# Performance work log

Measured on AMD Instinct MI355X. Metric: run time of the kernel, lower is better.

## Reference

```python
import jax, jax.numpy as jnp
import numpy as np


def setup_inputs() -> dict:
    key = jax.random.key(0)
    ks = jax.random.split(key, 4)
    C = 64
    return {
        "x": jax.random.normal(ks[0], (8, 64, 32, 32, 96), jnp.float32),
        "w_sr": jax.random.normal(ks[1], (64,), jnp.float32) * 0.1,
        "b_sr": jnp.zeros((64,), jnp.float32),
        "Wq": jax.random.normal(ks[2], (64, 64), jnp.float32) / np.sqrt(C),
        "bq": jnp.zeros((64,), jnp.float32),
        "Wkv": jax.random.normal(ks[3], (128, 64), jnp.float32) / np.sqrt(C),
        "bkv": jnp.zeros((128,), jnp.float32),
        "gamma": jnp.ones((4,), jnp.float32),
        "beta": jnp.zeros((4,), jnp.float32),
    }


def reference(x, w_sr, b_sr, Wq, bq, Wkv, bkv, gamma, beta):
    B, C, H, W, D = x.shape
    NH = gamma.shape[0]
    hd = C // NH
    scale = hd ** -0.5

    # 1x1x1 conv projections == channel matmuls
    q = jnp.einsum('oc,bchwd->bohwd', Wq, x) + bq[None, :, None, None, None]
    # sr_conv with sr_ratio=1 is a depthwise 1x1x1 conv: per-channel scale+shift
    kvin = x * w_sr[None, :, None, None, None] + b_sr[None, :, None, None, None]
    kv = jnp.einsum('oc,bchwd->bohwd', Wkv, kvin) + bkv[None, :, None, None, None]
    k, v = kv[:, :C], kv[:, C:]

    q = q.reshape(B, NH, hd, H, W, D)
    k = k.reshape(B, NH, hd, H, W, D)
    v = v.reshape(B, NH, hd, H, W, D)

    # Manhattan decay: spatial_dist[i,j] = |i-j| + |j-i| = 2|i-j| (H==W);
    # spectral_dist is identically zero in the original (d_idx.T is a no-op on 1D).
    idx = jnp.arange(H, dtype=x.dtype)
    dist = 2.0 * jnp.abs(idx[:, None] - idx[None, :])              # (H, H)
    dec = dist[None, :, :, None] * gamma[:, None, None, None] + beta[:, None, None, None]  # (NH,H,H,1)
    decay = jnp.exp(-jax.nn.softplus(dec))                          # broadcasts over D

    # matmul contracts over W; head_dim c is batch-like (faithful to original permutes)
    attn = jnp.einsum('bnchwd,bncgwd->bnchgd', q, k) * scale        # (B,NH,hd,H,H,D)
    attn = attn + decay[None, :, None]                               # (1,NH,1,H,H,1)
    attn = jax.nn.softmax(attn, axis=-1)                             # softmax over spectral D
    out = jnp.einsum('bnchgd,bncgjd->bnchjd', attn, v)               # (B,NH,hd,H,W,D)
    return out.reshape(B, C, H, W, D)
```

## Files before the change

kernel.cpp:

```cpp
#include <hip/hip_runtime.h>
#include <stdint.h>
#include <stddef.h>

typedef __attribute__((ext_vector_type(8))) short short8;
typedef __attribute__((ext_vector_type(4))) float f32x4;

#define PER_BO 98304
#define CSTRIDE 8192

__device__ __forceinline__ unsigned int cvtpk(float lo, float hi) {
    unsigned int r;
    asm("v_cvt_pk_bf16_f32 %0, %1, %2" : "=v"(r) : "v"(lo), "v"(hi));
    return r;
}

__global__ __launch_bounds__(512, 2) void proj_mfma(
    const float* __restrict__ x, const float* __restrict__ w_sr, const float* __restrict__ b_sr,
    const float* __restrict__ Wq, const float* __restrict__ bq,
    const float* __restrict__ Wkv, const float* __restrict__ bkv,
    unsigned short* __restrict__ qb, unsigned short* __restrict__ kb, unsigned short* __restrict__ vb)
{
    __shared__ unsigned short Wh[12288];
    __shared__ float bl[192];
    __shared__ unsigned short Cb[2 * 6464];

    int t = threadIdx.x;
    int bidx = blockIdx.x;
    int b = bidx >> 8;
    int blk = bidx & 255;

    int lane = t & 63;
    int wvi = t >> 6;
    int lr = lane & 15, hk = lane >> 4;

    const float* xb = x + (size_t)b * 6291456 + (size_t)blk * 384;
    float af[3][16];
#pragma unroll
    for (int pi = 0; pi < 3; ++pi) {
        int pt = wvi * 3 + pi;
        const float* xp = xb + (size_t)(hk * 8) * 98304 + pt * 16 + lr;
#pragma unroll
        for (int j = 0; j < 8; ++j) {
            af[pi][j]     = xp[(size_t)j * 98304];
            af[pi][8 + j] = xp[(size_t)(32 + j) * 98304];
        }
    }

#pragma unroll
    for (int i = 0; i < 6; ++i) {
        int qi = t + i * 512;
        int o = qi >> 4;
        int cq = qi & 15;
        int c = cq * 4;
        float4 wv4;
        if (o < 64) wv4 = *reinterpret_cast<const float4*>(Wq + o * 64 + c);
        else {
            wv4 = *reinterpret_cast<const float4*>(Wkv + (o - 64) * 64 + c);
            float4 sr = *reinterpret_cast<const float4*>(w_sr + c);
            wv4.x *= sr.x; wv4.y *= sr.y; wv4.z *= sr.z; wv4.w *= sr.w;
        }
        uint2 pk; pk.x = cvtpk(wv4.x, wv4.y); pk.y = cvtpk(wv4.z, wv4.w);
        int sw = (cq >> 1) ^ (o & 7);
        *reinterpret_cast<uint2*>(&Wh[o * 64 + sw * 8 + (cq & 1) * 4]) = pk;
    }
    if (t < 192) {
        float s;
        if (t < 64) s = bq[t];
        else {
            s = bkv[t - 64];
            for (int c = 0; c < 64; ++c) s += Wkv[(t - 64) * 64 + c] * b_sr[c];
        }
        bl[t] = s;
    }
    __syncthreads();

    short8 ahf[3][2], alf[3][2];
#pragma unroll
    for (int pi = 0; pi < 3; ++pi) {
#pragma unroll
        for (int half = 0; half < 2; ++half) {
            union { unsigned int u[4]; short8 v; } H, L;
#pragma unroll
            for (int q = 0; q < 4; ++q) {
                float f0 = af[pi][half * 8 + 2 * q];
                float f1 = af[pi][half * 8 + 2 * q + 1];
                unsigned int hp = cvtpk(f0, f1);
                float h0 = __uint_as_float(hp << 16);
                float h1 = __uint_as_float(hp & 0xffff0000u);
                H.u[q] = hp;
                L.u[q] = cvtpk(f0 - h0, f1 - h1);
            }
            ahf[pi][half] = H.v; alf[pi][half] = L.v;
        }
    }

    int wo[3];
#pragma unroll
    for (int pi = 0; pi < 3; ++pi) {
        int p0 = (wvi * 3 + pi) * 16 + hk * 4;
        int hwl = p0 / 96;
        int d0 = p0 - hwl * 96;
        wo[pi] = lr * 404 + hwl * 100 + d0;
    }

    int so_po[3], so_lo[3];
#pragma unroll
    for (int i = 0; i < 3; ++i) {
        int flat = i * 512 + t;
        int dlq = flat & 1;
        int hwl = (flat >> 1) & 3;
        int ch  = (flat >> 3) % 12;
        int o   = flat / 96;
        so_po[i] = o * PER_BO + ch * 8192 + (blk * 4 + hwl) * 8 + dlq * 4;
        so_lo[i] = o * 404 + hwl * 100 + ch * 8 + dlq * 4;
    }

    float biasv[12];
#pragma unroll
    for (int ot = 0; ot < 12; ++ot) biasv[ot] = bl[ot * 16 + lr];

    f32x4 zero4 = {0.f, 0.f, 0.f, 0.f};
    int s7 = lr & 7;

#pragma unroll
    for (int ot = 0; ot < 12; ++ot) {
        unsigned short* cb = Cb + (ot & 1) * 6464;
        {
            int o = ot * 16 + lr;
            const unsigned short* wr = &Wh[o * 64];
            short8 b0 = *reinterpret_cast<const short8*>(wr + ((hk ^ s7) * 8));
            short8 b1 = *reinterpret_cast<const short8*>(wr + (((hk + 4) ^ s7) * 8));
            float bo = biasv[ot];
#pragma unroll
            for (int pi = 0; pi < 3; ++pi) {
                f32x4 acc = __builtin_amdgcn_mfma_f32_16x16x32_bf16(ahf[pi][0], b0, zero4, 0, 0, 0);
                acc = __builtin_amdgcn_mfma_f32_16x16x32_bf16(ahf[pi][1], b1, acc, 0, 0, 0);
                acc = __builtin_amdgcn_mfma_f32_16x16x32_bf16(alf[pi][0], b0, acc, 0, 0, 0);
                acc = __builtin_amdgcn_mfma_f32_16x16x32_bf16(alf[pi][1], b1, acc, 0, 0, 0);
                uint2 st;
                st.x = cvtpk(acc[0] + bo, acc[1] + bo);
                st.y = cvtpk(acc[2] + bo, acc[3] + bo);
                *reinterpret_cast<uint2*>(&cb[wo[pi]]) = st;
            }
        }
        __syncthreads();
        {
            int sel = ot >> 2;
            unsigned short* base =
                (sel == 0 ? qb : (sel == 1 ? kb : vb)) + (size_t)(b * 64 + (ot & 3) * 16) * PER_BO;
#pragma unroll
            for (int i = 0; i < 3; ++i)
                *reinterpret_cast<uint2*>(base + so_po[i]) =
                    *reinterpret_cast<const uint2*>(&cb[so_lo[i]]);
        }
    }
}

__global__ __launch_bounds__(512, 4) void attn_kernel(
    const unsigned short* __restrict__ qb, const unsigned short* __restrict__ kb,
    const unsigned short* __restrict__ vb,
    const float* __restrict__ gamma, const float* __restrict__ beta,
    float* __restrict__ out)
{
    extern __shared__ char smem[];
    unsigned short* Qs = (unsigned short*)smem;
    unsigned short* Ks = (unsigned short*)(smem + 17408);
    float* lred = (float*)smem;
    float* rlb  = (float*)(smem + 16896);
    unsigned short* Vs = (unsigned short*)smem;
    float* Osf  = (float*)(smem + 34816);

    int t = threadIdx.x;
    int l = t & 63;
    int dsub = t >> 6;
    int lr = l & 15, hk = l >> 4;

    int id = blockIdx.x;
    int xcd = id & 7;
    int k7 = id >> 3;
    int p = xcd + 8 * (k7 >> 1);
    int half = k7 & 1;
    int oc = p & 63;
    int b = p >> 6;
    int n = oc >> 4;

    const unsigned short* qp = qb + (size_t)(b * 64 + oc) * PER_BO + half * 4096;
    const unsigned short* kp = kb + (size_t)(b * 64 + oc) * PER_BO;
    const unsigned short* vp = vb + (size_t)(b * 64 + oc) * PER_BO;

    float gm = gamma[n], bt = beta[n];
    float decv[8];
#pragma unroll
    for (int gb = 0; gb < 2; ++gb)
#pragma unroll
        for (int r = 0; r < 4; ++r) {
            int hh = half * 16 + hk * 4 + r;
            int gg = gb * 16 + lr;
            float dc = 2.0f * fabsf((float)(hh - gg)) * gm + bt;
            float sp = fmaxf(dc, 0.0f) + log1pf(__expf(-fabsf(dc)));
            decv[gb * 4 + r] = __expf(-sp);
        }

    const float scale = 0.25f;
    f32x4 zero4 = {0.f, 0.f, 0.f, 0.f};

    unsigned int ep[48];
    float lacc[8] = {0.f, 0.f, 0.f, 0.f, 0.f, 0.f, 0.f, 0.f};

    auto WRQ = [&](int buf, uint4 v) {
        const unsigned short* sq = (const unsigned short*)&v;
        int base = buf * 4352 + (t >> 5) * 34 + (t & 31);
#pragma unroll
        for (int i = 0; i < 8; ++i) Qs[base + i * 544] = sq[i];
    };
    auto WRK = [&](int buf, uint4 v0, uint4 v1) {
        const unsigned short* s0 = (const unsigned short*)&v0;
        const unsigned short* s1 = (const unsigned short*)&v1;
        int b0 = buf * 8704 + (t >> 5) * 34 + (t & 31);
        int b1 = buf * 8704 + ((t + 512) >> 5) * 34 + (t & 31);
#pragma unroll
        for (int i = 0; i < 8; ++i) { Ks[b0 + i * 1088] = s0[i]; Ks[b1 + i * 1088] = s1[i]; }
    };

    uint4 qh  = *reinterpret_cast<const uint4*>(qp + t * 8);
    uint4 kh0 = *reinterpret_cast<const uint4*>(kp + t * 8);
    uint4 kh1 = *reinterpret_cast<const uint4*>(kp + (t + 512) * 8);
    WRQ(0, qh); WRK(0, kh0, kh1);
    qh  = *reinterpret_cast<const uint4*>(qp + CSTRIDE + t * 8);
    kh0 = *reinterpret_cast<const uint4*>(kp + CSTRIDE + t * 8);
    kh1 = *reinterpret_cast<const uint4*>(kp + CSTRIDE + (t + 512) * 8);
    __syncthreads();

#pragma unroll
    for (int ch = 0; ch < 12; ++ch) {
        const unsigned short* qbase = Qs + (ch & 1) * 4352 + dsub * 544;
        const unsigned short* kbase = Ks + (ch & 1) * 8704 + dsub * 1088;
        short8 a  = *reinterpret_cast<const short8*>(qbase + lr * 34 + hk * 8);
        short8 b0 = *reinterpret_cast<const short8*>(kbase + lr * 34 + hk * 8);
        short8 b1 = *reinterpret_cast<const short8*>(kbase + (16 + lr) * 34 + hk * 8);
        f32x4 s0 = __builtin_amdgcn_mfma_f32_16x16x32_bf16(a, b0, zero4, 0, 0, 0);
        f32x4 s1 = __builtin_amdgcn_mfma_f32_16x16x32_bf16(a, b1, zero4, 0, 0, 0);
        float e[8];
#pragma unroll
        for (int r = 0; r < 4; ++r) {
            e[r]     = __expf(s0[r] * scale + decv[r]);
            e[4 + r] = __expf(s1[r] * scale + decv[4 + r]);
        }
#pragma unroll
        for (int i = 0; i < 8; ++i) lacc[i] += e[i];
        ep[ch * 4 + 0] = cvtpk(e[0], e[1]);
        ep[ch * 4 + 1] = cvtpk(e[2], e[3]);
        ep[ch * 4 + 2] = cvtpk(e[4], e[5]);
        ep[ch * 4 + 3] = cvtpk(e[6], e[7]);
        if (ch < 11) {
            WRQ((ch + 1) & 1, qh); WRK((ch + 1) & 1, kh0, kh1);
            if (ch < 10) {
                qh  = *reinterpret_cast<const uint4*>(qp + (ch + 2) * CSTRIDE + t * 8);
                kh0 = *reinterpret_cast<const uint4*>(kp + (ch + 2) * CSTRIDE + t * 8);
                kh1 = *reinterpret_cast<const uint4*>(kp + (ch + 2) * CSTRIDE + (t + 512) * 8);
            }
        }
        __syncthreads();
    }

#pragma unroll
    for (int i = 0; i < 8; ++i)
        lred[dsub * 528 + (hk * 4 + (i & 3)) * 33 + (i >> 2) * 16 + lr] = lacc[i];
    __syncthreads();
    {
        float rsum = 0.f;
#pragma unroll
        for (int s = 0; s < 8; ++s) rsum += lred[s * 528 + (t >> 5) * 33 + (t & 31)];
        rlb[(t >> 5) * 33 + (t & 31)] = 1.0f / rsum;
    }
    __syncthreads();
    float rl8[8];
#pragma unroll
    for (int i = 0; i < 8; ++i)
        rl8[i] = rlb[(hk * 4 + (i & 3)) * 33 + (i >> 2) * 16 + lr];
    __syncthreads();

    auto WRV = [&](int buf, uint4 v0, uint4 v1) {
        const unsigned short* s0 = (const unsigned short*)&v0;
        const unsigned short* s1 = (const unsigned short*)&v1;
        int a0 = buf * 8704 + (t & 31) * 34 + (t >> 5);
        int a1 = buf * 8704 + (t & 31) * 34 + (t >> 5) + 16;
#pragma unroll
        for (int i = 0; i < 8; ++i) { Vs[a0 + i * 1088] = s0[i]; Vs[a1 + i * 1088] = s1[i]; }
    };

    uint4 vh0 = *reinterpret_cast<const uint4*>(vp + t * 8);
    uint4 vh1 = *reinterpret_cast<const uint4*>(vp + (t + 512) * 8);
    WRV(0, vh0, vh1);
    vh0 = *reinterpret_cast<const uint4*>(vp + CSTRIDE + t * 8);
    vh1 = *reinterpret_cast<const uint4*>(vp + CSTRIDE + (t + 512) * 8);
    __syncthreads();

    unsigned short* Pb = (unsigned short*)(Osf + dsub * 528);
    size_t obase0 = ((size_t)(b * 64 + oc) * 1024 + half * 512 + t) * 96;
    float4 hA, hB;

#pragma unroll
    for (int ch = 0; ch < 12; ++ch) {
#pragma unroll
        for (int gb = 0; gb < 2; ++gb)
#pragma unroll
            for (int rp = 0; rp < 2; ++rp) {
                unsigned int u = ep[ch * 4 + gb * 2 + rp];
                float p0 = __uint_as_float(u << 16)         * rl8[gb * 4 + rp * 2];
                float p1 = __uint_as_float(u & 0xffff0000u) * rl8[gb * 4 + rp * 2 + 1];
                unsigned int pk = cvtpk(p0, p1);
                Pb[(hk * 4 + rp * 2) * 36 + gb * 16 + lr]     = (unsigned short)pk;
                Pb[(hk * 4 + rp * 2 + 1) * 36 + gb * 16 + lr] = (unsigned short)(pk >> 16);
            }
        asm volatile("s_waitcnt lgkmcnt(0)" ::: "memory");
        __builtin_amdgcn_sched_barrier(0);
        short8 pa = *reinterpret_cast<const short8*>(Pb + lr * 36 + hk * 8);
        const unsigned short* vbase = Vs + (ch & 1) * 8704 + dsub * 1088;
        short8 vb0 = *reinterpret_cast<const short8*>(vbase + lr * 34 + hk * 8);
        short8 vb1 = *reinterpret_cast<const short8*>(vbase + (16 + lr) * 34 + hk * 8);
        f32x4 o0 = __builtin_amdgcn_mfma_f32_16x16x32_bf16(pa, vb0, zero4, 0, 0, 0);
        f32x4 o1 = __builtin_amdgcn_mfma_f32_16x16x32_bf16(pa, vb1, zero4, 0, 0, 0);
        if (ch < 11) {
            WRV((ch + 1) & 1, vh0, vh1);
            if (ch < 10) {
                vh0 = *reinterpret_cast<const uint4*>(vp + (ch + 2) * CSTRIDE + t * 8);
                vh1 = *reinterpret_cast<const uint4*>(vp + (ch + 2) * CSTRIDE + (t + 512) * 8);
            }
        }
#pragma unroll
        for (int r = 0; r < 4; ++r) {
            Osf[dsub * 528 + (hk * 4 + r) * 33 + lr]      = o0[r];
            Osf[dsub * 528 + (hk * 4 + r) * 33 + 16 + lr] = o1[r];
        }
        __syncthreads();
        {
            int lidx = (t >> 5) * 33 + (t & 31);
            float4 cA, cB;
            cA.x = Osf[0 * 528 + lidx]; cA.y = Osf[1 * 528 + lidx];
            cA.z = Osf[2 * 528 + lidx]; cA.w = Osf[3 * 528 + lidx];
            cB.x = Osf[4 * 528 + lidx]; cB.y = Osf[5 * 528 + lidx];
            cB.z = Osf[6 * 528 + lidx]; cB.w = Osf[7 * 528 + lidx];
            if ((ch & 1) == 0) { hA = cA; hB = cB; }
            else {
                float* po = out + obase0 + (ch >> 1) * 16;
                *reinterpret_cast<float4*>(po)      = hA;
                *reinterpret_cast<float4*>(po + 4)  = hB;
                *reinterpret_cast<float4*>(po + 8)  = cA;
                *reinterpret_cast<float4*>(po + 12) = cB;
            }
        }
        __syncthreads();
    }
}

extern "C" void kernel_launch(void* const* d_in, const int* in_sizes, int n_in,
                              void* d_out, int out_size, void* d_ws, size_t ws_size,
                              hipStream_t stream) {
    const float* x     = (const float*)d_in[0];
    const float* w_sr  = (const float*)d_in[1];
    const float* b_sr  = (const float*)d_in[2];
    const float* Wq    = (const float*)d_in[3];
    const float* bq    = (const float*)d_in[4];
    const float* Wkv   = (const float*)d_in[5];
    const float* bkv   = (const float*)d_in[6];
    const float* gamma = (const float*)d_in[7];
    const float* beta  = (const float*)d_in[8];
    float* out = (float*)d_out;

    unsigned short* qb = (unsigned short*)d_ws;
    unsigned short* kb = qb + (size_t)50331648;
    unsigned short* vb = kb + (size_t)50331648;

    proj_mfma<<<2048, 512, 0, stream>>>(x, w_sr, b_sr, Wq, bq, Wkv, bkv, qb, kb, vb);

    (void)hipFuncSetAttribute(reinterpret_cast<const void*>(attn_kernel),
                              hipFuncAttributeMaxDynamicSharedMemorySize, 52224);
    attn_kernel<<<1024, 512, 52224, stream>>>(qb, kb, vb, gamma, beta, out);
}
```

Measured before the change: 298.4 us.

## Store projections in d-major fragment layout so attention loads MFMA operands directly

The projection kernel now writes q/k/v in a layout where the spectral index is outermost and the spatial position is contiguous, and it remaps block indices across XCDs. In the attention kernel, Q and K fragments are loaded from global memory straight into registers with a two-stage prefetch, which removes the shared-memory staging and the per-chunk barriers of the score phase. V is still transposed through per-wave shared memory, and output staging is double-buffered so a barrier is needed only every second chunk. The attention kernel also switches to larger static shared memory, which may lower occupancy, and the global loads become smaller and more scattered.

```diff
diff --git a/kernel.cpp b/kernel.cpp
--- a/kernel.cpp
+++ b/kernel.cpp
@@ -6,7 +6,6 @@
 typedef __attribute__((ext_vector_type(4))) float f32x4;
 
 #define PER_BO 98304
-#define CSTRIDE 8192
 
 __device__ __forceinline__ unsigned int cvtpk(float lo, float hi) {
     unsigned int r;
@@ -22,12 +21,13 @@
 {
     __shared__ unsigned short Wh[12288];
     __shared__ float bl[192];
-    __shared__ unsigned short Cb[2 * 6464];
+    __shared__ unsigned short Cb[2 * 6208];
 
     int t = threadIdx.x;
     int bidx = blockIdx.x;
-    int b = bidx >> 8;
-    int blk = bidx & 255;
+    int lf = (bidx & 7) * 256 + (bidx >> 3);
+    int b = lf >> 8;
+    int blk = lf & 255;
 
     int lane = t & 63;
     int wvi = t >> 6;
@@ -97,22 +97,20 @@
     int wo[3];
 #pragma unroll
     for (int pi = 0; pi < 3; ++pi) {
-        int p0 = (wvi * 3 + pi) * 16 + hk * 4;
-        int hwl = p0 / 96;
-        int d0 = p0 - hwl * 96;
-        wo[pi] = lr * 404 + hwl * 100 + d0;
+        int m0 = (wvi * 3 + pi) * 16 + hk * 4;
+        int hwl = m0 / 96;
+        int d0 = m0 - hwl * 96;
+        wo[pi] = lr * 388 + d0 * 4 + hwl;
     }
 
     int so_po[3], so_lo[3];
 #pragma unroll
     for (int i = 0; i < 3; ++i) {
         int flat = i * 512 + t;
-        int dlq = flat & 1;
-        int hwl = (flat >> 1) & 3;
-        int ch  = (flat >> 3) % 12;
-        int o   = flat / 96;
-        so_po[i] = o * PER_BO + ch * 8192 + (blk * 4 + hwl) * 8 + dlq * 4;
-        so_lo[i] = o * 404 + hwl * 100 + ch * 8 + dlq * 4;
+        int o_l = flat / 96;
+        int d = flat - o_l * 96;
+        so_po[i] = o_l * PER_BO + d * 1024 + blk * 4;
+        so_lo[i] = o_l * 388 + d * 4;
     }
 
     float biasv[12];
@@ -124,7 +122,7 @@
 
 #pragma unroll
     for (int ot = 0; ot < 12; ++ot) {
-        unsigned short* cb = Cb + (ot & 1) * 6464;
+        unsigned short* cb = Cb + (ot & 1) * 6208;
         {
             int o = ot * 16 + lr;
             const unsigned short* wr = &Wh[o * 64];
@@ -137,10 +135,12 @@
                 acc = __builtin_amdgcn_mfma_f32_16x16x32_bf16(ahf[pi][1], b1, acc, 0, 0, 0);
                 acc = __builtin_amdgcn_mfma_f32_16x16x32_bf16(alf[pi][0], b0, acc, 0, 0, 0);
                 acc = __builtin_amdgcn_mfma_f32_16x16x32_bf16(alf[pi][1], b1, acc, 0, 0, 0);
-                uint2 st;
-                st.x = cvtpk(acc[0] + bo, acc[1] + bo);
-                st.y = cvtpk(acc[2] + bo, acc[3] + bo);
-                *reinterpret_cast<uint2*>(&cb[wo[pi]]) = st;
+                unsigned int u0 = cvtpk(acc[0] + bo, acc[1] + bo);
+                unsigned int u1 = cvtpk(acc[2] + bo, acc[3] + bo);
+                cb[wo[pi]]      = (unsigned short)u0;
+                cb[wo[pi] + 4]  = (unsigned short)(u0 >> 16);
+                cb[wo[pi] + 8]  = (unsigned short)u1;
+                cb[wo[pi] + 12] = (unsigned short)(u1 >> 16);
             }
         }
         __syncthreads();
@@ -162,13 +162,12 @@
     const float* __restrict__ gamma, const float* __restrict__ beta,
     float* __restrict__ out)
 {
-    extern __shared__ char smem[];
-    unsigned short* Qs = (unsigned short*)smem;
-    unsigned short* Ks = (unsigned short*)(smem + 17408);
-    float* lred = (float*)smem;
-    float* rlb  = (float*)(smem + 16896);
-    unsigned short* Vs = (unsigned short*)smem;
-    float* Osf  = (float*)(smem + 34816);
+    __shared__ char smem[61440];
+    unsigned short* Vw = (unsigned short*)smem;
+    unsigned short* Pb = (unsigned short*)(smem + 18432);
+    float* Osf  = (float*)(smem + 27648);
+    float* lred = (float*)(smem + 27648);
+    float* rlb  = (float*)(smem + 27648 + 16896);
 
     int t = threadIdx.x;
     int l = t & 63;
@@ -184,7 +183,7 @@
     int b = p >> 6;
     int n = oc >> 4;
 
-    const unsigned short* qp = qb + (size_t)(b * 64 + oc) * PER_BO + half * 4096;
+    const unsigned short* qp = qb + (size_t)(b * 64 + oc) * PER_BO;
     const unsigned short* kp = kb + (size_t)(b * 64 + oc) * PER_BO;
     const unsigned short* vp = vb + (size_t)(b * 64 + oc) * PER_BO;
 
@@ -207,39 +206,35 @@
     unsigned int ep[48];
     float lacc[8] = {0.f, 0.f, 0.f, 0.f, 0.f, 0.f, 0.f, 0.f};
 
-    auto WRQ = [&](int buf, uint4 v) {
-        const unsigned short* sq = (const unsigned short*)&v;
-        int base = buf * 4352 + (t >> 5) * 34 + (t & 31);
-#pragma unroll
-        for (int i = 0; i < 8; ++i) Qs[base + i * 544] = sq[i];
-    };
-    auto WRK = [&](int buf, uint4 v0, uint4 v1) {
-        const unsigned short* s0 = (const unsigned short*)&v0;
-        const unsigned short* s1 = (const unsigned short*)&v1;
-        int b0 = buf * 8704 + (t >> 5) * 34 + (t & 31);
-        int b1 = buf * 8704 + ((t + 512) >> 5) * 34 + (t & 31);
-#pragma unroll
-        for (int i = 0; i < 8; ++i) { Ks[b0 + i * 1088] = s0[i]; Ks[b1 + i * 1088] = s1[i]; }
-    };
-
-    uint4 qh  = *reinterpret_cast<const uint4*>(qp + t * 8);
-    uint4 kh0 = *reinterpret_cast<const uint4*>(kp + t * 8);
-    uint4 kh1 = *reinterpret_cast<const uint4*>(kp + (t + 512) * 8);
-    WRQ(0, qh); WRK(0, kh0, kh1);
-    qh  = *reinterpret_cast<const uint4*>(qp + CSTRIDE + t * 8);
-    kh0 = *reinterpret_cast<const uint4*>(kp + CSTRIDE + t * 8);
-    kh1 = *reinterpret_cast<const uint4*>(kp + CSTRIDE + (t + 512) * 8);
-    __syncthreads();
+    int qoff  = half * 512 + lr * 32 + hk * 8;
+    int koff0 = lr * 32 + hk * 8;
+    int koff1 = koff0 + 512;
+
+    uint4 qv[2], k0v[2], k1v[2];
+    {
+        int b0p = dsub * 1024;
+        qv[0]  = *reinterpret_cast<const uint4*>(qp + b0p + qoff);
+        k0v[0] = *reinterpret_cast<const uint4*>(kp + b0p + koff0);
+        k1v[0] = *reinterpret_cast<const uint4*>(kp + b0p + koff1);
+        int b1p = (8 + dsub) * 1024;
+        qv[1]  = *reinterpret_cast<const uint4*>(qp + b1p + qoff);
+        k0v[1] = *reinterpret_cast<const uint4*>(kp + b1p + koff0);
+        k1v[1] = *reinterpret_cast<const uint4*>(kp + b1p + koff1);
+    }
 
 #pragma unroll
     for (int ch = 0; ch < 12; ++ch) {
-        const unsigned short* qbase = Qs + (ch & 1) * 4352 + dsub * 544;
-        const unsigned short* kbase = Ks + (ch & 1) * 8704 + dsub * 1088;
-        short8 a  = *reinterpret_cast<const short8*>(qbase + lr * 34 + hk * 8);
-        short8 b0 = *reinterpret_cast<const short8*>(kbase + lr * 34 + hk * 8);
-        short8 b1 = *reinterpret_cast<const short8*>(kbase + (16 + lr) * 34 + hk * 8);
-        f32x4 s0 = __builtin_amdgcn_mfma_f32_16x16x32_bf16(a, b0, zero4, 0, 0, 0);
-        f32x4 s1 = __builtin_amdgcn_mfma_f32_16x16x32_bf16(a, b1, zero4, 0, 0, 0);
+        int s = ch & 1;
+        union { uint4 u; short8 v; } A, B0, B1;
+        A.u = qv[s]; B0.u = k0v[s]; B1.u = k1v[s];
+        f32x4 s0 = __builtin_amdgcn_mfma_f32_16x16x32_bf16(A.v, B0.v, zero4, 0, 0, 0);
+        f32x4 s1 = __builtin_amdgcn_mfma_f32_16x16x32_bf16(A.v, B1.v, zero4, 0, 0, 0);
+        if (ch < 10) {
+            int bp = ((ch + 2) * 8 + dsub) * 1024;
+            qv[s]  = *reinterpret_cast<const uint4*>(qp + bp + qoff);
+            k0v[s] = *reinterpret_cast<const uint4*>(kp + bp + koff0);
+            k1v[s] = *reinterpret_cast<const uint4*>(kp + bp + koff1);
+        }
         float e[8];
 #pragma unroll
         for (int r = 0; r < 4; ++r) {
@@ -252,15 +247,6 @@
         ep[ch * 4 + 1] = cvtpk(e[2], e[3]);
         ep[ch * 4 + 2] = cvtpk(e[4], e[5]);
         ep[ch * 4 + 3] = cvtpk(e[6], e[7]);
-        if (ch < 11) {
-            WRQ((ch + 1) & 1, qh); WRK((ch + 1) & 1, kh0, kh1);
-            if (ch < 10) {
-                qh  = *reinterpret_cast<const uint4*>(qp + (ch + 2) * CSTRIDE + t * 8);
-                kh0 = *reinterpret_cast<const uint4*>(kp + (ch + 2) * CSTRIDE + t * 8);
-                kh1 = *reinterpret_cast<const uint4*>(kp + (ch + 2) * CSTRIDE + (t + 512) * 8);
-            }
-        }
-        __syncthreads();
     }
 
 #pragma unroll
@@ -280,28 +266,33 @@
         rl8[i] = rlb[(hk * 4 + (i & 3)) * 33 + (i >> 2) * 16 + lr];
     __syncthreads();
 
-    auto WRV = [&](int buf, uint4 v0, uint4 v1) {
-        const unsigned short* s0 = (const unsigned short*)&v0;
-        const unsigned short* s1 = (const unsigned short*)&v1;
-        int a0 = buf * 8704 + (t & 31) * 34 + (t >> 5);
-        int a1 = buf * 8704 + (t & 31) * 34 + (t >> 5) + 16;
-#pragma unroll
-        for (int i = 0; i < 8; ++i) { Vs[a0 + i * 1088] = s0[i]; Vs[a1 + i * 1088] = s1[i]; }
-    };
-
-    uint4 vh0 = *reinterpret_cast<const uint4*>(vp + t * 8);
-    uint4 vh1 = *reinterpret_cast<const uint4*>(vp + (t + 512) * 8);
-    WRV(0, vh0, vh1);
-    vh0 = *reinterpret_cast<const uint4*>(vp + CSTRIDE + t * 8);
-    vh1 = *reinterpret_cast<const uint4*>(vp + CSTRIDE + (t + 512) * 8);
-    __syncthreads();
-
-    unsigned short* Pb = (unsigned short*)(Osf + dsub * 528);
+    int vgoff = l * 16;
+    int vwbase = dsub * 1152 + ((l & 1) * 16) * 36 + (l >> 1);
+    unsigned short* Pw = Pb + dsub * 576;
+
+    uint4 vv0[2], vv1[2];
+    {
+        int b0p = dsub * 1024 + vgoff;
+        vv0[0] = *reinterpret_cast<const uint4*>(vp + b0p);
+        vv1[0] = *reinterpret_cast<const uint4*>(vp + b0p + 8);
+        int b1p = (8 + dsub) * 1024 + vgoff;
+        vv0[1] = *reinterpret_cast<const uint4*>(vp + b1p);
+        vv1[1] = *reinterpret_cast<const uint4*>(vp + b1p + 8);
+    }
+
     size_t obase0 = ((size_t)(b * 64 + oc) * 1024 + half * 512 + t) * 96;
-    float4 hA, hB;
 
 #pragma unroll
     for (int ch = 0; ch < 12; ++ch) {
+        int s = ch & 1;
+        {
+            union { uint4 u; unsigned short e[8]; } V0, V1;
+            V0.u = vv0[s]; V1.u = vv1[s];
+#pragma unroll
+            for (int i = 0; i < 8; ++i) Vw[vwbase + i * 36] = V0.e[i];
+#pragma unroll
+            for (int i = 0; i < 8; ++i) Vw[vwbase + (i + 8) * 36] = V1.e[i];
+        }
 #pragma unroll
         for (int gb = 0; gb < 2; ++gb)
 #pragma unroll
@@ -310,47 +301,46 @@
                 float p0 = __uint_as_float(u << 16)         * rl8[gb * 4 + rp * 2];
                 float p1 = __uint_as_float(u & 0xffff0000u) * rl8[gb * 4 + rp * 2 + 1];
                 unsigned int pk = cvtpk(p0, p1);
-                Pb[(hk * 4 + rp * 2) * 36 + gb * 16 + lr]     = (unsigned short)pk;
-                Pb[(hk * 4 + rp * 2 + 1) * 36 + gb * 16 + lr] = (unsigned short)(pk >> 16);
+                Pw[(hk * 4 + rp * 2) * 36 + gb * 16 + lr]     = (unsigned short)pk;
+                Pw[(hk * 4 + rp * 2 + 1) * 36 + gb * 16 + lr] = (unsigned short)(pk >> 16);
             }
+        if (ch < 10) {
+            int bp = ((ch + 2) * 8 + dsub) * 1024 + vgoff;
+            vv0[s] = *reinterpret_cast<const uint4*>(vp + bp);
+            vv1[s] = *reinterpret_cast<const uint4*>(vp + bp + 8);
+        }
         asm volatile("s_waitcnt lgkmcnt(0)" ::: "memory");
         __builtin_amdgcn_sched_barrier(0);
-        short8 pa = *reinterpret_cast<const short8*>(Pb + lr * 36 + hk * 8);
-        const unsigned short* vbase = Vs + (ch & 1) * 8704 + dsub * 1088;
-        short8 vb0 = *reinterpret_cast<const short8*>(vbase + lr * 34 + hk * 8);
-        short8 vb1 = *reinterpret_cast<const short8*>(vbase + (16 + lr) * 34 + hk * 8);
+        short8 pa  = *reinterpret_cast<const short8*>(Pw + lr * 36 + hk * 8);
+        short8 vb0 = *reinterpret_cast<const short8*>(Vw + dsub * 1152 + lr * 36 + hk * 8);
+        short8 vb1 = *reinterpret_cast<const short8*>(Vw + dsub * 1152 + (16 + lr) * 36 + hk * 8);
         f32x4 o0 = __builtin_amdgcn_mfma_f32_16x16x32_bf16(pa, vb0, zero4, 0, 0, 0);
         f32x4 o1 = __builtin_amdgcn_mfma_f32_16x16x32_bf16(pa, vb1, zero4, 0, 0, 0);
-        if (ch < 11) {
-            WRV((ch + 1) & 1, vh0, vh1);
-            if (ch < 10) {
-                vh0 = *reinterpret_cast<const uint4*>(vp + (ch + 2) * CSTRIDE + t * 8);
-                vh1 = *reinterpret_cast<const uint4*>(vp + (ch + 2) * CSTRIDE + (t + 512) * 8);
-            }
-        }
+        float* Od = Osf + s * 4224 + dsub * 528;
 #pragma unroll
         for (int r = 0; r < 4; ++r) {
-            Osf[dsub * 528 + (hk * 4 + r) * 33 + lr]      = o0[r];
-            Osf[dsub * 528 + (hk * 4 + r) * 33 + 16 + lr] = o1[r];
-        }
-        __syncthreads();
-        {
+            Od[(hk * 4 + r) * 33 + lr]      = o0[r];
+            Od[(hk * 4 + r) * 33 + 16 + lr] = o1[r];
+        }
+        if (ch & 1) {
+            __syncthreads();
             int lidx = (t >> 5) * 33 + (t & 31);
-            float4 cA, cB;
-            cA.x = Osf[0 * 528 + lidx]; cA.y = Osf[1 * 528 + lidx];
-            cA.z = Osf[2 * 528 + lidx]; cA.w = Osf[3 * 528 + lidx];
-            cB.x = Osf[4 * 528 + lidx]; cB.y = Osf[5 * 528 + lidx];
-            cB.z = Osf[6 * 528 + lidx]; cB.w = Osf[7 * 528 + lidx];
-            if ((ch & 1) == 0) { hA = cA; hB = cB; }
-            else {
-                float* po = out + obase0 + (ch >> 1) * 16;
-                *reinterpret_cast<float4*>(po)      = hA;
-                *reinterpret_cast<float4*>(po + 4)  = hB;
-                *reinterpret_cast<float4*>(po + 8)  = cA;
-                *reinterpret_cast<float4*>(po + 12) = cB;
-            }
-        }
-        __syncthreads();
+            float4 q0, q1, q2, q3;
+            q0.x = Osf[0 * 528 + lidx]; q0.y = Osf[1 * 528 + lidx];
+            q0.z = Osf[2 * 528 + lidx]; q0.w = Osf[3 * 528 + lidx];
+            q1.x = Osf[4 * 528 + lidx]; q1.y = Osf[5 * 528 + lidx];
+            q1.z = Osf[6 * 528 + lidx]; q1.w = Osf[7 * 528 + lidx];
+            q2.x = Osf[4224 + 0 * 528 + lidx]; q2.y = Osf[4224 + 1 * 528 + lidx];
+            q2.z = Osf[4224 + 2 * 528 + lidx]; q2.w = Osf[4224 + 3 * 528 + lidx];
+            q3.x = Osf[4224 + 4 * 528 + lidx]; q3.y = Osf[4224 + 5 * 528 + lidx];
+            q3.z = Osf[4224 + 6 * 528 + lidx]; q3.w = Osf[4224 + 7 * 528 + lidx];
+            float* po = out + obase0 + (ch >> 1) * 16;
+            *reinterpret_cast<float4*>(po)      = q0;
+            *reinterpret_cast<float4*>(po + 4)  = q1;
+            *reinterpret_cast<float4*>(po + 8)  = q2;
+            *reinterpret_cast<float4*>(po + 12) = q3;
+            __syncthreads();
+        }
     }
 }
 
@@ -374,7 +364,5 @@
 
     proj_mfma<<<2048, 512, 0, stream>>>(x, w_sr, b_sr, Wq, bq, Wkv, bkv, qb, kb, vb);
 
-    (void)hipFuncSetAttribute(reinterpret_cast<const void*>(attn_kernel),
-                              hipFuncAttributeMaxDynamicSharedMemorySize, 52224);
-    attn_kernel<<<1024, 512, 52224, stream>>>(qb, kb, vb, gamma, beta, out);
+    attn_kernel<<<1024, 512, 0, stream>>>(qb, kb, vb, gamma, beta, out);
 }
```

Result: slower. 462.8 us (+55.1%).
